# Performance work log

Measured on AMD Instinct MI355X. Metric: run time of the kernel, lower is better.

## Reference

```python
import jax, jax.numpy as jnp
import numpy as np

K = 7          # kernel_size
PAD = K // 2   # padding


def _unfold(t):
    """im2col for kxk neighborhood: (B,C,H,W) -> (B,C,K*K,H,W), zero-padded."""
    B, C, H, W = t.shape
    p = jnp.pad(t, ((0, 0), (0, 0), (PAD, PAD), (PAD, PAD)))
    # row-major over kernel offsets matches F.unfold ordering
    wins = jnp.stack([p[:, :, i:i + H, j:j + W]
                      for i in range(K) for j in range(K)], axis=2)
    return wins


def setup_inputs() -> dict:
    key = jax.random.key(0)
    ks = jax.random.split(key, 7)
    B, C, H, W = 8, 128, 64, 64
    scale = 1.0 / np.sqrt(C)
    x = jax.random.normal(ks[0], (B, C, H, W), dtype=jnp.float32)
    Wq = jax.random.normal(ks[1], (C, C), dtype=jnp.float32) * scale
    Wk = jax.random.normal(ks[2], (C, C), dtype=jnp.float32) * scale
    Wv = jax.random.normal(ks[3], (C, C), dtype=jnp.float32) * scale
    bq = jax.random.normal(ks[4], (C,), dtype=jnp.float32) * 0.01
    bk = jax.random.normal(ks[5], (C,), dtype=jnp.float32) * 0.01
    bv = jax.random.normal(ks[6], (C,), dtype=jnp.float32) * 0.01
    return {"x": x, "Wq": Wq, "bq": bq, "Wk": Wk, "bk": bk, "Wv": Wv, "bv": bv}


def reference(x, Wq, bq, Wk, bk, Wv, bv):
    # 1x1 convs = channel GEMMs
    q = jnp.einsum('oc,bchw->bohw', Wq, x) + bq[:, None, None]
    k = jnp.einsum('oc,bchw->bohw', Wk, x) + bk[:, None, None]
    v = jnp.einsum('oc,bchw->bohw', Wv, x) + bv[:, None, None]
    k_unf = _unfold(k)   # (B,C,K*K,H,W)
    v_unf = _unfold(v)   # (B,C,K*K,H,W)
    # attention scores over the K*K neighborhood, summed over channels
    attn = jnp.einsum('bchw,bcphw->bphw', q, k_unf)
    attn = jax.nn.softmax(attn, axis=1)
    y = jnp.einsum('bphw,bcphw->bchw', attn, v_unf)
    return y
```

## Files before the change

### kernel.cpp

```cpp
#include <hip/hip_runtime.h>
#include <hip/hip_bf16.h>

#define CC   128
#define HH_  64
#define WW_  64
#define BB   8
#define HWSZ (HH_*WW_)
#define CHW  (CC*HWSZ)
#define BCHW (BB*CHW)
#define PAD  3
#define NP   49

typedef __attribute__((ext_vector_type(8))) short short8;
typedef __attribute__((ext_vector_type(4))) float float4v;

__global__ __launch_bounds__(256) void prep_w(
    const float* __restrict__ Wq, const float* __restrict__ Wk,
    const float* __restrict__ Wv,
    unsigned short* __restrict__ whi, unsigned short* __restrict__ wlo)
{
    int i = blockIdx.x * 256 + threadIdx.x;
    const float* src = (i < 16384) ? Wq : (i < 32768 ? Wk : Wv);
    float f = src[i & 16383];
    __hip_bfloat16 h = __float2bfloat16(f);
    float hf = __bfloat162float(h);
    __hip_bfloat16 l = __float2bfloat16(f - hf);
    unsigned short hu, lu;
    __builtin_memcpy(&hu, &h, 2);
    __builtin_memcpy(&lu, &l, 2);
    whi[i] = hu;
    wlo[i] = lu;
}

__global__ __launch_bounds__(256, 2) void qkv_mfma(
    const float* __restrict__ x,
    const unsigned short* __restrict__ whi, const unsigned short* __restrict__ wlo,
    const float* __restrict__ bq, const float* __restrict__ bk,
    const float* __restrict__ bv, float* __restrict__ qkv)
{
    __shared__ unsigned short xT[2][128][136];
    const int proj = blockIdx.y;
    const int n0g  = blockIdx.x << 7;
    const int b    = n0g >> 12;
    const int npx  = n0g & 4095;
    const int tid  = threadIdx.x;
    const int lane = tid & 63;
    const int wv   = tid >> 6;
    const int wm   = wv & 1, wn = wv >> 1;

    const float* xb = x + (size_t)b*CHW + npx;
    #pragma unroll
    for (int it = 0; it < 16; ++it) {
        int f  = tid + (it << 8);
        int c  = f >> 5;
        int p4 = (f & 31) << 2;
        float4 v = *(const float4*)&xb[(size_t)c*HWSZ + p4];
        float vv[4] = {v.x, v.y, v.z, v.w};
        #pragma unroll
        for (int u = 0; u < 4; ++u) {
            __hip_bfloat16 h = __float2bfloat16(vv[u]);
            float hf = __bfloat162float(h);
            __hip_bfloat16 l = __float2bfloat16(vv[u] - hf);
            unsigned short hu, lu;
            __builtin_memcpy(&hu, &h, 2);
            __builtin_memcpy(&lu, &l, 2);
            xT[0][p4 + u][c] = hu;
            xT[1][p4 + u][c] = lu;
        }
    }

    const float* Bp = (proj == 0) ? bq : (proj == 1 ? bk : bv);
    const int q4 = lane >> 4;
    float4v acc[4][4];
    #pragma unroll
    for (int sm = 0; sm < 4; ++sm) {
        const int mb = wm*64 + sm*16 + q4*4;
        float4v bi;
        bi[0] = Bp[mb+0]; bi[1] = Bp[mb+1]; bi[2] = Bp[mb+2]; bi[3] = Bp[mb+3];
        #pragma unroll
        for (int sn = 0; sn < 4; ++sn) acc[sm][sn] = bi;
    }

    __syncthreads();

    const unsigned short* Wh = whi + (size_t)proj*16384;
    const unsigned short* Wl = wlo + (size_t)proj*16384;
    const int kq8  = q4 << 3;
    const int mrow = lane & 15;

    for (int pass = 0; pass < 3; ++pass) {
        const unsigned short* Wp = (pass == 2) ? Wl : Wh;
        const int xi = (pass == 1) ? 1 : 0;
        #pragma unroll
        for (int kc = 0; kc < 4; ++kc) {
            const int kb = kc << 5;
            short8 a[4], bf[4];
            #pragma unroll
            for (int sm = 0; sm < 4; ++sm) {
                const int m = wm*64 + sm*16 + mrow;
                a[sm] = *(const short8*)&Wp[(size_t)m*CC + kb + kq8];
            }
            #pragma unroll
            for (int sn = 0; sn < 4; ++sn) {
                const int n = wn*64 + sn*16 + mrow;
                bf[sn] = *(const short8*)&xT[xi][n][kb + kq8];
            }
            #pragma unroll
            for (int sm = 0; sm < 4; ++sm)
                #pragma unroll
                for (int sn = 0; sn < 4; ++sn)
                    acc[sm][sn] = __builtin_amdgcn_mfma_f32_16x16x32_bf16(
                        a[sm], bf[sn], acc[sm][sn], 0, 0, 0);
        }
    }

    float* op = qkv + (size_t)proj*BCHW + (size_t)b*CHW + npx;
    #pragma unroll
    for (int sm = 0; sm < 4; ++sm) {
        const int mb = wm*64 + sm*16 + q4*4;
        #pragma unroll
        for (int sn = 0; sn < 4; ++sn) {
            const int n = wn*64 + sn*16 + mrow;
            #pragma unroll
            for (int r = 0; r < 4; ++r)
                op[(size_t)(mb + r)*HWSZ + n] = acc[sm][sn][r];
        }
    }
}

__device__ __forceinline__ void load_chunk7(const float* __restrict__ src,
                                            int h, int c0, float4* stg) {
    const int tid = threadIdx.x;
    #pragma unroll
    for (int i = 0; i < 4; ++i) {
        int f   = tid + (i << 9);
        int c   = f >> 7;
        int rem = f & 127;
        int r   = rem >> 4;
        int q4  = (rem & 15) << 2;
        int hh  = h - PAD + r;
        if (r < 7 && (unsigned)hh < (unsigned)HH_)
            stg[i] = *(const float4*)&src[(size_t)(c0 + c)*HWSZ + hh*WW_ + q4];
        else
            stg[i] = make_float4(0.f, 0.f, 0.f, 0.f);
    }
}

__global__ __launch_bounds__(512, 4) void locatt(
    const float* __restrict__ qkv, float* __restrict__ out)
{
    __shared__ __align__(16) float smem[16*8*72];
    __shared__ float lg[NP][64];
    __shared__ float dn[64];

    const int blk = blockIdx.x;
    const int xs  = blk & 7;
    const int jj  = blk >> 3;
    const int b   = jj >> 3;
    const int h   = (xs << 3) | (jj & 7);
    const int tid = threadIdx.x;
    const int s    = tid >> 6;
    const int lane = tid & 63;
    const int q16  = lane & 15;
    const int csub = lane >> 4;
    const int w4   = q16 << 2;
    const int w    = lane;

    const float* qp = qkv + (size_t)b*CHW;
    const float* kp = qkv + (size_t)BCHW + (size_t)b*CHW;
    const float* vp = qkv + (size_t)2*BCHW + (size_t)b*CHW;

    float (*ks)[8][72] = (float(*)[8][72])smem;

    if (tid < 256) {
        int idx = tid & 127;
        int c = idx >> 3, r = idx & 7;
        int col = (tid < 128) ? 0 : 68;
        *(float4*)&ks[c][r][col] = make_float4(0.f, 0.f, 0.f, 0.f);
    }

    const bool activeA = (s < 7);

    float acc[7][4];
    #pragma unroll
    for (int dx = 0; dx < 7; ++dx)
        #pragma unroll
        for (int j = 0; j < 4; ++j) acc[dx][j] = 0.f;

    float4 stg[4];
    load_chunk7(kp, h, 0, stg);

    for (int ck = 0; ck < 8; ++ck) {
        #pragma unroll
        for (int i = 0; i < 4; ++i) {
            int f   = tid + (i << 9);
            int c   = f >> 7;
            int rem = f & 127;
            int r   = rem >> 4;
            int q4  = (rem & 15) << 2;
            *(float4*)&ks[c][r][4 + q4] = stg[i];
        }
        __syncthreads();
        if (ck < 7) load_chunk7(kp, h, (ck + 1) * 16, stg);

        if (activeA) {
            const int c0 = ck << 4;
            #pragma unroll
            for (int ci4 = 0; ci4 < 4; ++ci4) {
                const int c = (ci4 << 2) + csub;
                const float* qc = qp + (size_t)(c0 + c)*HWSZ
                                     + (size_t)h*WW_ + w4;
                float4 qv  = *(const float4*)qc;
                float4 ka  = *(const float4*)&ks[c][s][w4];
                float4 kb  = *(const float4*)&ks[c][s][w4 + 4];
                float4 kc2 = *(const float4*)&ks[c][s][w4 + 8];
                float kw[12] = {ka.x,ka.y,ka.z,ka.w, kb.x,kb.y,kb.z,kb.w,
                                kc2.x,kc2.y,kc2.z,kc2.w};
                float qa[4] = {qv.x,qv.y,qv.z,qv.w};
                #pragma unroll
                for (int dx = 0; dx < 7; ++dx)
                    #pragma unroll
                    for (int j = 0; j < 4; ++j) {
                        float kv = kw[j + dx + 1];
                        acc[dx][j] = fmaf(qa[j], kv, acc[dx][j]);
                    }
            }
        }
        __syncthreads();
    }

    if (activeA) {
        #pragma unroll
        for (int dx = 0; dx < 7; ++dx)
            #pragma unroll
            for (int j = 0; j < 4; ++j) {
                acc[dx][j] += __shfl_xor(acc[dx][j], 16, 64);
                acc[dx][j] += __shfl_xor(acc[dx][j], 32, 64);
            }
        const int p0 = s * 7;
        #pragma unroll
        for (int dx = 0; dx < 7; ++dx) {
            if ((dx & 3) == csub)
                *(float4*)&lg[p0 + dx][w4] =
                    make_float4(acc[dx][0], acc[dx][1], acc[dx][2], acc[dx][3]);
        }
    }

    const int cpl = s << 1;
    float vreg[14];
    {
        #pragma unroll
        for (int i = 0; i < 14; ++i) {
            int ch = (i >= 7) ? 1 : 0;
            int r  = i - 7*ch;
            int hh = h - PAD + r;
            vreg[i] = ((unsigned)hh < (unsigned)HH_)
                      ? vp[(size_t)(cpl + ch)*HWSZ + hh*WW_ + w] : 0.f;
        }
    }
    __syncthreads();

    if (tid < 64) {
        const int px = tid;
        float tv[NP];
        float m = -1e30f;
        #pragma unroll
        for (int p = 0; p < NP; ++p) { tv[p] = lg[p][px]; m = fmaxf(m, tv[p]); }
        float d = 0.f;
        #pragma unroll
        for (int p = 0; p < NP; ++p) {
            float e = __expf(tv[p] - m);
            d += e;
            lg[p][px] = e;
        }
        dn[px] = 1.f / d;
    } else {
        int t = tid - 64;
        for (int i = t; i < 896; i += 448) {
            int r    = i >> 7;
            int rem  = i & 127;
            int colg = rem >> 4;
            int col  = (colg < 4) ? colg : (64 + colg);
            smem[r*1224 + col*17 + (rem & 15)] = 0.f;
        }
    }
    __syncthreads();

    float a[NP];
    const float sc = dn[w];
    #pragma unroll
    for (int p = 0; p < NP; ++p) a[p] = lg[p][w] * sc;

    for (int ck = 0; ck < 8; ++ck) {
        #pragma unroll
        for (int i = 0; i < 14; ++i) {
            int ch = (i >= 7) ? 1 : 0;
            int r  = i - 7*ch;
            smem[r*1224 + (4 + w)*17 + cpl + ch] = vreg[i];
        }
        __syncthreads();
        if (ck < 7) {
            int c0v = (ck + 1) << 4;
            #pragma unroll
            for (int i = 0; i < 14; ++i) {
                int ch = (i >= 7) ? 1 : 0;
                int r  = i - 7*ch;
                int hh = h - PAD + r;
                vreg[i] = ((unsigned)hh < (unsigned)HH_)
                          ? vp[(size_t)(c0v + cpl + ch)*HWSZ + hh*WW_ + w] : 0.f;
            }
        }
        float ya = 0.f, yb = 0.f;
        #pragma unroll
        for (int r = 0; r < 7; ++r) {
            const float* vbase = &smem[r*1224 + (1 + w)*17 + cpl];
            #pragma unroll
            for (int dx = 0; dx < 7; ++dx) {
                float va = vbase[17*dx];
                float vb = vbase[17*dx + 1];
                float aw = a[r*7 + dx];
                ya = fmaf(aw, va, ya);
                yb = fmaf(aw, vb, yb);
            }
        }
        float* op = out + (size_t)b*CHW + (size_t)(ck*16 + cpl)*HWSZ
                        + (size_t)h*WW_ + w;
        op[0]    = ya;
        op[HWSZ] = yb;
        __syncthreads();
    }
}

extern "C" void kernel_launch(void* const* d_in, const int* in_sizes, int n_in,
                              void* d_out, int out_size, void* d_ws, size_t ws_size,
                              hipStream_t stream) {
    const float* x  = (const float*)d_in[0];
    const float* Wq = (const float*)d_in[1];
    const float* bq = (const float*)d_in[2];
    const float* Wk = (const float*)d_in[3];
    const float* bk = (const float*)d_in[4];
    const float* Wv = (const float*)d_in[5];
    const float* bv = (const float*)d_in[6];
    float* out = (float*)d_out;
    float* qkv = (float*)d_ws;

    unsigned short* whi = (unsigned short*)d_out;
    unsigned short* wlo = whi + 3*16384;

    prep_w  <<<192, 256, 0, stream>>>(Wq, Wk, Wv, whi, wlo);
    qkv_mfma<<<dim3(256, 3), 256, 0, stream>>>(x, whi, wlo, bq, bk, bv, qkv);
    locatt  <<<512, 512, 0, stream>>>(qkv, out);
}
```

Measured before the change: 151.7 us.

## Swizzle xT LDS layout and restructure AV phase to reuse logit-style tiling

The projection kernel now XOR-swizzles the channel index of the transposed bf16 x tile in shared memory, so the MFMA B-operand reads avoid LDS bank conflicts. In the attention kernel, the value-aggregation phase switches to the same float4-per-lane layout used for the logits. Each lane handles 4 pixels across 2 neighbourhood rows and loads V with load_chunk7 into the ks tile. Partial sums are combined with cross-lane shuffles, and the softmax normalisation is applied at store time. This drops the 49-register attention array and the scalar strided LDS reads, at the cost of extra shuffles, a padded logits buffer, and stores from only half the lanes.

```diff
diff --git a/kernel.cpp b/kernel.cpp
--- a/kernel.cpp
+++ b/kernel.cpp
@@ -54,6 +54,7 @@
         int f  = tid + (it << 8);
         int c  = f >> 5;
         int p4 = (f & 31) << 2;
+        int csw = (((c >> 3) ^ ((p4 >> 3) & 7)) << 3) | (c & 7);
         float4 v = *(const float4*)&xb[(size_t)c*HWSZ + p4];
         float vv[4] = {v.x, v.y, v.z, v.w};
         #pragma unroll
@@ -64,8 +65,8 @@
             unsigned short hu, lu;
             __builtin_memcpy(&hu, &h, 2);
             __builtin_memcpy(&lu, &l, 2);
-            xT[0][p4 + u][c] = hu;
-            xT[1][p4 + u][c] = lu;
+            xT[0][p4 + u][csw] = hu;
+            xT[1][p4 + u][csw] = lu;
         }
     }
 
@@ -103,7 +104,8 @@
             #pragma unroll
             for (int sn = 0; sn < 4; ++sn) {
                 const int n = wn*64 + sn*16 + mrow;
-                bf[sn] = *(const short8*)&xT[xi][n][kb + kq8];
+                const int scol = (kb + kq8) ^ (((n >> 3) & 7) << 3);
+                bf[sn] = *(const short8*)&xT[xi][n][scol];
             }
             #pragma unroll
             for (int sm = 0; sm < 4; ++sm)
@@ -150,7 +152,7 @@
     const float* __restrict__ qkv, float* __restrict__ out)
 {
     __shared__ __align__(16) float smem[16*8*72];
-    __shared__ float lg[NP][64];
+    __shared__ float lg[56][64];
     __shared__ float dn[64];
 
     const int blk = blockIdx.x;
@@ -164,7 +166,6 @@
     const int q16  = lane & 15;
     const int csub = lane >> 4;
     const int w4   = q16 << 2;
-    const int w    = lane;
 
     const float* qp = qkv + (size_t)b*CHW;
     const float* kp = qkv + (size_t)BCHW + (size_t)b*CHW;
@@ -246,18 +247,7 @@
         }
     }
 
-    const int cpl = s << 1;
-    float vreg[14];
-    {
-        #pragma unroll
-        for (int i = 0; i < 14; ++i) {
-            int ch = (i >= 7) ? 1 : 0;
-            int r  = i - 7*ch;
-            int hh = h - PAD + r;
-            vreg[i] = ((unsigned)hh < (unsigned)HH_)
-                      ? vp[(size_t)(cpl + ch)*HWSZ + hh*WW_ + w] : 0.f;
-        }
-    }
+    load_chunk7(vp, h, 0, stg);
     __syncthreads();
 
     if (tid < 64) {
@@ -276,57 +266,80 @@
         dn[px] = 1.f / d;
     } else {
         int t = tid - 64;
-        for (int i = t; i < 896; i += 448) {
-            int r    = i >> 7;
-            int rem  = i & 127;
-            int colg = rem >> 4;
-            int col  = (colg < 4) ? colg : (64 + colg);
-            smem[r*1224 + col*17 + (rem & 15)] = 0.f;
-        }
+        lg[49 + (t >> 6)][t & 63] = 0.f;
     }
     __syncthreads();
 
-    float a[NP];
-    const float sc = dn[w];
-    #pragma unroll
-    for (int p = 0; p < NP; ++p) a[p] = lg[p][w] * sc;
-
+    float4v av[14];
+    #pragma unroll
+    for (int i = 0; i < 14; ++i)
+        av[i] = *(const float4v*)&lg[14*csub + i][w4];
+    const float4 dnv = *(const float4*)&dn[w4];
+
+    const int cA = s << 1, cB = (s << 1) + 1;
     for (int ck = 0; ck < 8; ++ck) {
         #pragma unroll
-        for (int i = 0; i < 14; ++i) {
-            int ch = (i >= 7) ? 1 : 0;
-            int r  = i - 7*ch;
-            smem[r*1224 + (4 + w)*17 + cpl + ch] = vreg[i];
+        for (int i = 0; i < 4; ++i) {
+            int f   = tid + (i << 9);
+            int c   = f >> 7;
+            int rem = f & 127;
+            int r   = rem >> 4;
+            int q4  = (rem & 15) << 2;
+            *(float4*)&ks[c][r][4 + q4] = stg[i];
         }
         __syncthreads();
-        if (ck < 7) {
-            int c0v = (ck + 1) << 4;
-            #pragma unroll
-            for (int i = 0; i < 14; ++i) {
-                int ch = (i >= 7) ? 1 : 0;
-                int r  = i - 7*ch;
-                int hh = h - PAD + r;
-                vreg[i] = ((unsigned)hh < (unsigned)HH_)
-                          ? vp[(size_t)(c0v + cpl + ch)*HWSZ + hh*WW_ + w] : 0.f;
-            }
-        }
-        float ya = 0.f, yb = 0.f;
-        #pragma unroll
-        for (int r = 0; r < 7; ++r) {
-            const float* vbase = &smem[r*1224 + (1 + w)*17 + cpl];
-            #pragma unroll
-            for (int dx = 0; dx < 7; ++dx) {
-                float va = vbase[17*dx];
-                float vb = vbase[17*dx + 1];
-                float aw = a[r*7 + dx];
-                ya = fmaf(aw, va, ya);
-                yb = fmaf(aw, vb, yb);
-            }
-        }
-        float* op = out + (size_t)b*CHW + (size_t)(ck*16 + cpl)*HWSZ
-                        + (size_t)h*WW_ + w;
-        op[0]    = ya;
-        op[HWSZ] = yb;
+        if (ck < 7) load_chunk7(vp, h, (ck + 1) * 16, stg);
+
+        float accA[4] = {0.f, 0.f, 0.f, 0.f};
+        float accB[4] = {0.f, 0.f, 0.f, 0.f};
+        #pragma unroll
+        for (int rl = 0; rl < 2; ++rl) {
+            const int r = (csub << 1) + rl;
+            {
+                float4 ka  = *(const float4*)&ks[cA][r][w4];
+                float4 kb  = *(const float4*)&ks[cA][r][w4 + 4];
+                float4 kc2 = *(const float4*)&ks[cA][r][w4 + 8];
+                float vw[12] = {ka.x,ka.y,ka.z,ka.w, kb.x,kb.y,kb.z,kb.w,
+                                kc2.x,kc2.y,kc2.z,kc2.w};
+                #pragma unroll
+                for (int dx = 0; dx < 7; ++dx)
+                    #pragma unroll
+                    for (int j = 0; j < 4; ++j)
+                        accA[j] = fmaf(av[rl*7 + dx][j], vw[j + dx + 1], accA[j]);
+            }
+            {
+                float4 ka  = *(const float4*)&ks[cB][r][w4];
+                float4 kb  = *(const float4*)&ks[cB][r][w4 + 4];
+                float4 kc2 = *(const float4*)&ks[cB][r][w4 + 8];
+                float vw[12] = {ka.x,ka.y,ka.z,ka.w, kb.x,kb.y,kb.z,kb.w,
+                                kc2.x,kc2.y,kc2.z,kc2.w};
+                #pragma unroll
+                for (int dx = 0; dx < 7; ++dx)
+                    #pragma unroll
+                    for (int j = 0; j < 4; ++j)
+                        accB[j] = fmaf(av[rl*7 + dx][j], vw[j + dx + 1], accB[j]);
+            }
+        }
+        float fin[4];
+        #pragma unroll
+        for (int j = 0; j < 4; ++j) {
+            accA[j] += __shfl_xor(accA[j], 32, 64);
+            accB[j] += __shfl_xor(accB[j], 32, 64);
+        }
+        #pragma unroll
+        for (int j = 0; j < 4; ++j) {
+            float sel  = (csub & 1) ? accA[j] : accB[j];
+            float oth  = __shfl_xor(sel, 16, 64);
+            float mine = (csub & 1) ? accB[j] : accA[j];
+            fin[j] = mine + oth;
+        }
+        if (csub < 2) {
+            const int cg = (ck << 4) + ((s << 1) | csub);
+            float4 o = make_float4(fin[0]*dnv.x, fin[1]*dnv.y,
+                                   fin[2]*dnv.z, fin[3]*dnv.w);
+            *(float4*)&out[(size_t)b*CHW + (size_t)cg*HWSZ
+                           + (size_t)h*WW_ + w4] = o;
+        }
         __syncthreads();
     }
 }
```

Measured after the change: 156.3 us. 3.0% more time.

## Precompute bf16 hi/lo split of x once and stream it into LDS directly

Applied to the files above, without the earlier changes.

Adds a prep_x kernel that transposes x to pixel-major layout and splits it into bf16 hi/lo halves with an XOR swizzle, written once to workspace. The QKV GEMM kernel then loads these tiles with global_load_lds instead of converting x separately in each of the three projection blocks. This removes the triplicated conversion and the strided LDS transpose stores, at the cost of an extra kernel launch and an extra round trip of 8 MB of bf16 data through global memory.

```diff
diff --git a/kernel.cpp b/kernel.cpp
--- a/kernel.cpp
+++ b/kernel.cpp
@@ -13,6 +13,13 @@
 
 typedef __attribute__((ext_vector_type(8))) short short8;
 typedef __attribute__((ext_vector_type(4))) float float4v;
+
+__device__ __forceinline__ void gload16(const unsigned short* g, unsigned short* l) {
+    __builtin_amdgcn_global_load_lds(
+        (const __attribute__((address_space(1))) void*)(g),
+        (__attribute__((address_space(3))) void*)(l),
+        16, 0, 0);
+}
 
 __global__ __launch_bounds__(256) void prep_w(
     const float* __restrict__ Wq, const float* __restrict__ Wk,
@@ -32,13 +39,53 @@
     wlo[i] = lu;
 }
 
+__global__ __launch_bounds__(256) void prep_x(
+    const float* __restrict__ x, unsigned short* __restrict__ xhi,
+    unsigned short* __restrict__ xlo)
+{
+    __shared__ float xt[128][132];
+    const int b   = blockIdx.x >> 5;
+    const int p0  = (blockIdx.x & 31) << 7;
+    const int tid = threadIdx.x;
+    const float* xb = x + (size_t)b*CHW + p0;
+    #pragma unroll
+    for (int i = 0; i < 16; ++i) {
+        int f  = tid + (i << 8);
+        int c  = f >> 5;
+        int q4 = (f & 31) << 2;
+        *(float4*)&xt[c][q4] = *(const float4*)&xb[(size_t)c*HWSZ + q4];
+    }
+    __syncthreads();
+    const int px  = tid >> 1;
+    const int jb0 = (tid & 1) << 3;
+    unsigned short* oh = xhi + (size_t)b*(size_t)(HWSZ*CC) + (size_t)(p0 + px)*CC;
+    unsigned short* ol = xlo + (size_t)b*(size_t)(HWSZ*CC) + (size_t)(p0 + px)*CC;
+    #pragma unroll
+    for (int j = 0; j < 8; ++j) {
+        int jb = jb0 + j;
+        int pb = jb ^ (px & 7);
+        unsigned short hs[8], ls[8];
+        #pragma unroll
+        for (int e = 0; e < 8; ++e) {
+            float f = xt[jb*8 + e][px];
+            __hip_bfloat16 h = __float2bfloat16(f);
+            float hf = __bfloat162float(h);
+            __hip_bfloat16 l = __float2bfloat16(f - hf);
+            __builtin_memcpy(&hs[e], &h, 2);
+            __builtin_memcpy(&ls[e], &l, 2);
+        }
+        *(short8*)&oh[pb << 3] = *(short8*)hs;
+        *(short8*)&ol[pb << 3] = *(short8*)ls;
+    }
+}
+
 __global__ __launch_bounds__(256, 2) void qkv_mfma(
-    const float* __restrict__ x,
+    const unsigned short* __restrict__ xhi, const unsigned short* __restrict__ xlo,
     const unsigned short* __restrict__ whi, const unsigned short* __restrict__ wlo,
     const float* __restrict__ bq, const float* __restrict__ bk,
     const float* __restrict__ bv, float* __restrict__ qkv)
 {
-    __shared__ unsigned short xT[2][128][136];
+    __shared__ unsigned short xs[2][128][128];
     const int proj = blockIdx.y;
     const int n0g  = blockIdx.x << 7;
     const int b    = n0g >> 12;
@@ -48,25 +95,13 @@
     const int wv   = tid >> 6;
     const int wm   = wv & 1, wn = wv >> 1;
 
-    const float* xb = x + (size_t)b*CHW + npx;
-    #pragma unroll
-    for (int it = 0; it < 16; ++it) {
-        int f  = tid + (it << 8);
-        int c  = f >> 5;
-        int p4 = (f & 31) << 2;
-        float4 v = *(const float4*)&xb[(size_t)c*HWSZ + p4];
-        float vv[4] = {v.x, v.y, v.z, v.w};
-        #pragma unroll
-        for (int u = 0; u < 4; ++u) {
-            __hip_bfloat16 h = __float2bfloat16(vv[u]);
-            float hf = __bfloat162float(h);
-            __hip_bfloat16 l = __float2bfloat16(vv[u] - hf);
-            unsigned short hu, lu;
-            __builtin_memcpy(&hu, &h, 2);
-            __builtin_memcpy(&lu, &l, 2);
-            xT[0][p4 + u][c] = hu;
-            xT[1][p4 + u][c] = lu;
-        }
+    const unsigned short* xh = xhi + (size_t)b*(size_t)(HWSZ*CC) + (size_t)npx*CC;
+    const unsigned short* xl = xlo + (size_t)b*(size_t)(HWSZ*CC) + (size_t)npx*CC;
+    #pragma unroll
+    for (int i = 0; i < 8; ++i) {
+        int ch = (i << 8) + tid;
+        gload16(xh + ch*8, &xs[0][0][0] + ch*8);
+        gload16(xl + ch*8, &xs[1][0][0] + ch*8);
     }
 
     const float* Bp = (proj == 0) ? bq : (proj == 1 ? bk : bv);
@@ -103,7 +138,8 @@
             #pragma unroll
             for (int sn = 0; sn < 4; ++sn) {
                 const int n = wn*64 + sn*16 + mrow;
-                bf[sn] = *(const short8*)&xT[xi][n][kb + kq8];
+                const int pblk = ((kc << 2) | q4) ^ (mrow & 7);
+                bf[sn] = *(const short8*)&xs[xi][n][pblk << 3];
             }
             #pragma unroll
             for (int sm = 0; sm < 4; ++sm)
@@ -344,10 +380,14 @@
     float* out = (float*)d_out;
     float* qkv = (float*)d_ws;
 
+    unsigned short* xhi = (unsigned short*)((char*)d_ws + (size_t)3*BCHW*4);
+    unsigned short* xlo = xhi + (size_t)BCHW;
+
     unsigned short* whi = (unsigned short*)d_out;
     unsigned short* wlo = whi + 3*16384;
 
     prep_w  <<<192, 256, 0, stream>>>(Wq, Wk, Wv, whi, wlo);
-    qkv_mfma<<<dim3(256, 3), 256, 0, stream>>>(x, whi, wlo, bq, bk, bv, qkv);
+    prep_x  <<<256, 256, 0, stream>>>(x, xhi, xlo);
+    qkv_mfma<<<dim3(256, 3), 256, 0, stream>>>(xhi, xlo, whi, wlo, bq, bk, bv, qkv);
     locatt  <<<512, 512, 0, stream>>>(qkv, out);
 }
```

Result: no change. 153.5 us (+1.2%).
